# Kernel optimization log

Hardware: AMD Instinct MI355X
Metric: run time of the kernel (lower is better)

The kernel has to match this reference:

```python
import jax, jax.numpy as jnp
import numpy as np

B, S, D, H = 2, 2048, 1024, 16
DK = D // H  # 64

def setup_inputs() -> dict:
    key = jax.random.key(0)
    ks = jax.random.split(key, 8)
    xavier = np.sqrt(6.0 / (D + D))  # xavier_uniform bound for square Linear
    def lin_w(k):
        return jax.random.uniform(k, (D, D), jnp.float32, -xavier, xavier)
    return {
        'Q': jax.random.normal(ks[0], (B, S, D), jnp.float32),
        'length': jax.random.randint(ks[1], (B,), 1, S + 1, jnp.int32),
        'Wq': lin_w(ks[2]), 'bq': jnp.zeros((D,), jnp.float32),
        'Wk': lin_w(ks[3]), 'bk': jnp.zeros((D,), jnp.float32),
        'Wv': lin_w(ks[4]), 'bv': jnp.zeros((D,), jnp.float32),
    }

def reference(Q, length, Wq, bq, Wk, bk, Wv, bv):
    # project and split heads: [B,S,D] -> [B,H,S,DK]
    def heads(x, W, b):
        y = jnp.einsum('bsd,de->bse', x, W) + b
        return y.reshape(B, S, H, DK).transpose(0, 2, 1, 3)
    q = heads(Q, Wq, bq)
    k = heads(Q, Wk, bk)
    v = heads(Q, Wv, bv)
    scores = jnp.einsum('bhqd,bhkd->bhqk', q, k) / np.sqrt(DK)
    scores = jnp.exp(scores)  # NOTE: raw exp, no max-subtraction (faithful)
    # multiplicative key mask: mask[b,k] = k < length[b], broadcast over q,h
    mask = (jnp.arange(S)[None, :] < length[:, None]).astype(scores.dtype)
    scores = scores * mask[:, None, None, :]
    attn = scores / (jnp.sum(scores, axis=-1, keepdims=True) + 1e-8)
    ctx = jnp.einsum('bhqk,bhkd->bhqd', attn, v)
    return ctx.transpose(0, 2, 1, 3).reshape(B, S, D)
```

## Files before the change

### kernel.cpp

```cpp
#include <hip/hip_runtime.h>
#include <hip/hip_bf16.h>

#define B_  2
#define S_  2048
#define D_  1024
#define H_  16
#define DK_ 64
#define M_  (B_ * S_)

typedef short short8 __attribute__((ext_vector_type(8)));
typedef float float4v __attribute__((ext_vector_type(4)));

#define QSCALE 0.18033688011112042f

static __device__ __forceinline__ ushort f32_to_bf16bits(float f) {
    union { __hip_bfloat16 h; ushort u; } cv;
    cv.h = __float2bfloat16(f);
    return cv.u;
}

static __device__ __forceinline__ void glds16(const ushort* g, ushort* l) {
    __builtin_amdgcn_global_load_lds(
        (const __attribute__((address_space(1))) unsigned int*)g,
        (__attribute__((address_space(3))) unsigned int*)l, 16, 0, 0);
}

__global__ __launch_bounds__(256) void prep(
    const float* __restrict__ X, const float* __restrict__ W0,
    const float* __restrict__ W1, const float* __restrict__ W2,
    ushort* __restrict__ Xb, ushort* __restrict__ Wt)
{
    const int z = blockIdx.z;
    const int t = threadIdx.x;

    if (z >= 3) {
        const int blk = (z - 3) * 256 + blockIdx.y * 16 + blockIdx.x;
        const int i = blk * 2048 + t * 8;
        float4v a = *(const float4v*)(X + i);
        float4v b = *(const float4v*)(X + i + 4);
        short8 o;
        o[0] = (short)f32_to_bf16bits(a[0]); o[1] = (short)f32_to_bf16bits(a[1]);
        o[2] = (short)f32_to_bf16bits(a[2]); o[3] = (short)f32_to_bf16bits(a[3]);
        o[4] = (short)f32_to_bf16bits(b[0]); o[5] = (short)f32_to_bf16bits(b[1]);
        o[6] = (short)f32_to_bf16bits(b[2]); o[7] = (short)f32_to_bf16bits(b[3]);
        *(short8*)(Xb + i) = o;
        return;
    }

    const float* W = (z == 0) ? W0 : ((z == 1) ? W1 : W2);
    ushort* out = Wt + (size_t)z * D_ * D_;

    __shared__ ushort tile[64 * 72];
    int n0 = blockIdx.x * 64, k0 = blockIdx.y * 64;
    int r = t >> 3, g = t & 7;

    #pragma unroll
    for (int p = 0; p < 2; ++p) {
        int rr = r + p * 32;
        const float* src = W + (size_t)(k0 + rr) * D_ + n0 + g * 8;
        float4v a = *(const float4v*)src;
        float4v b = *(const float4v*)(src + 4);
        short8 o;
        o[0] = (short)f32_to_bf16bits(a[0]); o[1] = (short)f32_to_bf16bits(a[1]);
        o[2] = (short)f32_to_bf16bits(a[2]); o[3] = (short)f32_to_bf16bits(a[3]);
        o[4] = (short)f32_to_bf16bits(b[0]); o[5] = (short)f32_to_bf16bits(b[1]);
        o[6] = (short)f32_to_bf16bits(b[2]); o[7] = (short)f32_to_bf16bits(b[3]);
        *(short8*)&tile[rr * 72 + g * 8] = o;
    }
    __syncthreads();
    #pragma unroll
    for (int p = 0; p < 2; ++p) {
        int rr = r + p * 32;
        short8 v;
        #pragma unroll
        for (int i = 0; i < 8; ++i)
            v[i] = (short)tile[(g * 8 + i) * 72 + rr];
        *(short8*)(out + (size_t)(n0 + rr) * D_ + k0 + g * 8) = v;
    }
}

__global__ __launch_bounds__(256, 2) void proj_gemm(
    const ushort* __restrict__ X,
    const ushort* __restrict__ Wt,
    const float* __restrict__ b0, const float* __restrict__ b1,
    const float* __restrict__ b2,
    const int* __restrict__ length,
    ushort* __restrict__ qkv)
{
    const int m0 = blockIdx.x * 64, n0 = blockIdx.y * 128;
    const int bidx = m0 >> 11;
    const int s0 = m0 & (S_ - 1);
    const bool kv = (s0 < length[bidx]);

    __shared__ __align__(16) ushort As[64 * 64];
    __shared__ __align__(16) ushort Bs[3][128 * 64];

    const int t = threadIdx.x;
    const int lane = t & 63, wid = t >> 6;
    const int quad = lane >> 4, l16 = lane & 15;
    const int wr = wid >> 1, wc = wid & 1;

    float4v accq[2][4] = {}, acck[2][4] = {}, accv[2][4] = {};

    for (int kt = 0; kt < 16; ++kt) {
        const int k0 = kt * 64;
        __syncthreads();
        #pragma unroll
        for (int j = 0; j < 2; ++j) {
            const int cid = wid * 128 + j * 64 + lane;
            const int row = cid >> 3;
            const int cl  = (cid & 7) ^ (row & 7);
            glds16(X + (size_t)(m0 + row) * D_ + k0 + cl * 8, &As[cid * 8]);
        }
        #pragma unroll
        for (int j = 0; j < 4; ++j) {
            const int cid = wid * 256 + j * 64 + lane;
            const int row = cid >> 3;
            const int cl  = (cid & 7) ^ (row & 7);
            const size_t off = (size_t)(n0 + row) * D_ + k0 + cl * 8;
            glds16(Wt + off, &Bs[0][cid * 8]);
            if (kv) {
                glds16(Wt + (size_t)D_ * D_ + off,     &Bs[1][cid * 8]);
                glds16(Wt + (size_t)2 * D_ * D_ + off, &Bs[2][cid * 8]);
            }
        }
        __syncthreads();

        #pragma unroll
        for (int ks = 0; ks < 2; ++ks) {
            short8 a[2];
            #pragma unroll
            for (int i = 0; i < 2; ++i) {
                const int r = wr * 32 + i * 16 + l16;
                const int ph = (ks * 4 + quad) ^ (r & 7);
                a[i] = *(short8*)&As[r * 64 + ph * 8];
            }
            short8 bq[4];
            #pragma unroll
            for (int j = 0; j < 4; ++j) {
                const int r = wc * 64 + j * 16 + l16;
                const int ph = (ks * 4 + quad) ^ (r & 7);
                bq[j] = *(short8*)&Bs[0][r * 64 + ph * 8];
            }
            #pragma unroll
            for (int i = 0; i < 2; ++i)
                #pragma unroll
                for (int j = 0; j < 4; ++j)
                    accq[i][j] = __builtin_amdgcn_mfma_f32_16x16x32_bf16(
                        a[i], bq[j], accq[i][j], 0, 0, 0);
            if (kv) {
                short8 bk[4], bv[4];
                #pragma unroll
                for (int j = 0; j < 4; ++j) {
                    const int r = wc * 64 + j * 16 + l16;
                    const int ph = (ks * 4 + quad) ^ (r & 7);
                    bk[j] = *(short8*)&Bs[1][r * 64 + ph * 8];
                    bv[j] = *(short8*)&Bs[2][r * 64 + ph * 8];
                }
                #pragma unroll
                for (int i = 0; i < 2; ++i)
                    #pragma unroll
                    for (int j = 0; j < 4; ++j) {
                        acck[i][j] = __builtin_amdgcn_mfma_f32_16x16x32_bf16(
                            a[i], bk[j], acck[i][j], 0, 0, 0);
                        accv[i][j] = __builtin_amdgcn_mfma_f32_16x16x32_bf16(
                            a[i], bv[j], accv[i][j], 0, 0, 0);
                    }
            }
        }
    }

    #pragma unroll
    for (int j = 0; j < 4; ++j) {
        const int col = n0 + wc * 64 + j * 16 + l16;
        const int h = col >> 6, dk = col & (DK_ - 1);
        const float bvq = b0[col], bvk = b1[col], bvv = b2[col];
        #pragma unroll
        for (int i = 0; i < 2; ++i) {
            #pragma unroll
            for (int rr = 0; rr < 4; ++rr) {
                const int row = m0 + wr * 32 + i * 16 + quad * 4 + rr;
                const int s = row & (S_ - 1);
                const size_t hdr = ((size_t)(bidx * H_ + h) * S_ + s) * DK_ + dk;
                qkv[hdr] = f32_to_bf16bits((accq[i][j][rr] + bvq) * QSCALE);
                if (kv) {
                    qkv[(size_t)M_ * D_ + hdr] =
                        f32_to_bf16bits(acck[i][j][rr] + bvk);
                    qkv[(size_t)2 * M_ * D_ +
                        ((size_t)(bidx * H_ + h) * DK_ + dk) * S_ + s] =
                        f32_to_bf16bits(accv[i][j][rr] + bvv);
                }
            }
        }
    }
}

__global__ __launch_bounds__(256, 3) void attention(
    const ushort* __restrict__ qkv, const int* __restrict__ length,
    float* __restrict__ out)
{
    const int b = blockIdx.z, h = blockIdx.y, q0 = blockIdx.x * 64;
    int len = length[b];
    if (len > S_) len = S_;
    if (len < 1) len = 1;
    const int nkt = (len + 63) >> 6;

    const ushort* qb = qkv + ((size_t)(b * H_ + h) * S_ + q0) * DK_;
    const ushort* kb = qkv + (size_t)M_ * D_ + (size_t)(b * H_ + h) * S_ * DK_;
    const ushort* vb = qkv + (size_t)2 * M_ * D_ + (size_t)(b * H_ + h) * DK_ * S_;

    __shared__ __align__(16) ushort Qs[64 * 64];
    __shared__ __align__(16) ushort Ks[2][64 * 64];
    __shared__ __align__(16) ushort Vs[2][64 * 64];
    __shared__ __align__(16) ushort Ps[64 * 64];

    const int t = threadIdx.x, lane = t & 63, wid = t >> 6;
    const int quad = lane >> 4, l16 = lane & 15;
    const int qrow = wid * 16 + l16;
    const int e8 = (l16 & 7) << 1;

    #pragma unroll
    for (int j = 0; j < 2; ++j) {
        const int cid = wid * 128 + j * 64 + lane;
        const int row = cid >> 3;
        const int cl  = (cid & 7) ^ (row & 7);
        glds16(qb + (size_t)row * DK_ + cl * 8, &Qs[cid * 8]);
        glds16(kb + (size_t)row * DK_ + cl * 8, &Ks[0][cid * 8]);
        glds16(vb + (size_t)row * S_ + cl * 8,  &Vs[0][cid * 8]);
    }
    __syncthreads();

    short8 qfrag[2];
    #pragma unroll
    for (int ks = 0; ks < 2; ++ks) {
        const int phb = (ks * 4 + quad) ^ (l16 & 7);
        qfrag[ks] = *(short8*)&Qs[qrow * 64 + phb * 8];
    }

    short8 ones8;
    #pragma unroll
    for (int i = 0; i < 8; ++i) ones8[i] = (short)0x3F80;

    float4v cacc[4] = {};
    float4v racc = {};

    for (int kt = 0; kt < nkt; ++kt) {
        const int cur = kt & 1, nxt = cur ^ 1;
        if (kt + 1 < nkt) {
            #pragma unroll
            for (int j = 0; j < 2; ++j) {
                const int cid = wid * 128 + j * 64 + lane;
                const int row = cid >> 3;
                const int cl  = (cid & 7) ^ (row & 7);
                glds16(kb + (size_t)((kt + 1) * 64 + row) * DK_ + cl * 8,
                       &Ks[nxt][cid * 8]);
                glds16(vb + (size_t)row * S_ + (kt + 1) * 64 + cl * 8,
                       &Vs[nxt][cid * 8]);
            }
        }

        float4v sacc[4] = {};
        #pragma unroll
        for (int ks = 0; ks < 2; ++ks) {
            #pragma unroll
            for (int ct = 0; ct < 4; ++ct) {
                const int krow = ct * 16 + l16;
                const int pha = (ks * 4 + quad) ^ (krow & 7);
                short8 ak = *(short8*)&Ks[cur][krow * 64 + pha * 8];
                sacc[ct] = __builtin_amdgcn_mfma_f32_16x16x32_bf16(
                    ak, qfrag[ks], sacc[ct], 0, 0, 0);
            }
        }

        const bool full = ((kt + 1) * 64 <= len);
        #pragma unroll
        for (int ct = 0; ct < 4; ++ct) {
            float v0 = __builtin_amdgcn_exp2f(sacc[ct][0]);
            float v1 = __builtin_amdgcn_exp2f(sacc[ct][1]);
            float v2 = __builtin_amdgcn_exp2f(sacc[ct][2]);
            float v3 = __builtin_amdgcn_exp2f(sacc[ct][3]);
            if (!full) {
                const int kb0 = kt * 64 + ct * 16 + quad * 4;
                v0 = (kb0 + 0 < len) ? v0 : 0.f;
                v1 = (kb0 + 1 < len) ? v1 : 0.f;
                v2 = (kb0 + 2 < len) ? v2 : 0.f;
                v3 = (kb0 + 3 < len) ? v3 : 0.f;
            }
            uint2 w;
            w.x = (__float_as_uint(v0) >> 16) | (__float_as_uint(v1) & 0xFFFF0000u);
            w.y = (__float_as_uint(v2) >> 16) | (__float_as_uint(v3) & 0xFFFF0000u);
            const int c8 = (ct * 4 + quad) ^ e8;
            *(uint2*)&Ps[qrow * 64 + c8 * 4] = w;
        }

        #pragma unroll
        for (int ks = 0; ks < 2; ++ks) {
            const int pp = ((ks * 4 + quad) * 2) ^ e8;
            short8 ap = *(short8*)&Ps[qrow * 64 + pp * 4];
            #pragma unroll
            for (int ct = 0; ct < 4; ++ct) {
                const int vrow = ct * 16 + l16;
                const int phv = (ks * 4 + quad) ^ (vrow & 7);
                short8 vv = *(short8*)&Vs[cur][vrow * 64 + phv * 8];
                cacc[ct] = __builtin_amdgcn_mfma_f32_16x16x32_bf16(
                    ap, vv, cacc[ct], 0, 0, 0);
            }
            racc = __builtin_amdgcn_mfma_f32_16x16x32_bf16(
                ap, ones8, racc, 0, 0, 0);
        }
        __syncthreads();
    }

    #pragma unroll
    for (int rr = 0; rr < 4; ++rr) {
        const float inv = 1.0f / (racc[rr] + 1e-8f);
        const int q = q0 + wid * 16 + quad * 4 + rr;
        #pragma unroll
        for (int ct = 0; ct < 4; ++ct) {
            const int d = h * 64 + ct * 16 + l16;
            out[((size_t)b * S_ + q) * D_ + d] = cacc[ct][rr] * inv;
        }
    }
}

extern "C" void kernel_launch(void* const* d_in, const int* in_sizes, int n_in,
                              void* d_out, int out_size, void* d_ws, size_t ws_size,
                              hipStream_t stream)
{
    const float* Q   = (const float*)d_in[0];
    const int*   len = (const int*)d_in[1];
    const float* Wq  = (const float*)d_in[2];
    const float* bq  = (const float*)d_in[3];
    const float* Wk  = (const float*)d_in[4];
    const float* bk  = (const float*)d_in[5];
    const float* Wv  = (const float*)d_in[6];
    const float* bv  = (const float*)d_in[7];
    float* out = (float*)d_out;

    ushort* ws  = (ushort*)d_ws;
    ushort* Xb  = ws;
    ushort* Wt  = ws + (size_t)M_ * D_;
    ushort* qkv = Wt + (size_t)3 * D_ * D_;

    dim3 gPr(16, 16, 11);
    prep<<<gPr, 256, 0, stream>>>(Q, Wq, Wk, Wv, Xb, Wt);

    dim3 gP(M_ / 64, D_ / 128);
    proj_gemm<<<gP, 256, 0, stream>>>(Xb, Wt, bq, bk, bv, len, qkv);

    dim3 gA(S_ / 64, H_, B_);
    attention<<<gA, 256, 0, stream>>>(qkv, len, out);
}
```

Measured before the change: 156.2 us.

## Shrink projection tiles, alias Q/P shared memory, and interleave attention grid order

```diff
diff --git a/kernel.cpp b/kernel.cpp
--- a/kernel.cpp
+++ b/kernel.cpp
@@ -79,7 +79,7 @@
     }
 }
 
-__global__ __launch_bounds__(256, 2) void proj_gemm(
+__global__ __launch_bounds__(256, 4) void proj_gemm(
     const ushort* __restrict__ X,
     const ushort* __restrict__ Wt,
     const float* __restrict__ b0, const float* __restrict__ b1,
@@ -87,20 +87,22 @@
     const int* __restrict__ length,
     ushort* __restrict__ qkv)
 {
-    const int m0 = blockIdx.x * 64, n0 = blockIdx.y * 128;
+    const int bx = blockIdx.x;
+    const int m0 = (bx & 63) * 64;
+    const int n0 = (bx >> 6) * 64;
     const int bidx = m0 >> 11;
     const int s0 = m0 & (S_ - 1);
     const bool kv = (s0 < length[bidx]);
 
     __shared__ __align__(16) ushort As[64 * 64];
-    __shared__ __align__(16) ushort Bs[3][128 * 64];
+    __shared__ __align__(16) ushort Bs[3][64 * 64];
 
     const int t = threadIdx.x;
     const int lane = t & 63, wid = t >> 6;
     const int quad = lane >> 4, l16 = lane & 15;
     const int wr = wid >> 1, wc = wid & 1;
 
-    float4v accq[2][4] = {}, acck[2][4] = {}, accv[2][4] = {};
+    float4v accq[2][2] = {}, acck[2][2] = {}, accv[2][2] = {};
 
     for (int kt = 0; kt < 16; ++kt) {
         const int k0 = kt * 64;
@@ -111,12 +113,6 @@
             const int row = cid >> 3;
             const int cl  = (cid & 7) ^ (row & 7);
             glds16(X + (size_t)(m0 + row) * D_ + k0 + cl * 8, &As[cid * 8]);
-        }
-        #pragma unroll
-        for (int j = 0; j < 4; ++j) {
-            const int cid = wid * 256 + j * 64 + lane;
-            const int row = cid >> 3;
-            const int cl  = (cid & 7) ^ (row & 7);
             const size_t off = (size_t)(n0 + row) * D_ + k0 + cl * 8;
             glds16(Wt + off, &Bs[0][cid * 8]);
             if (kv) {
@@ -135,24 +131,24 @@
                 const int ph = (ks * 4 + quad) ^ (r & 7);
                 a[i] = *(short8*)&As[r * 64 + ph * 8];
             }
-            short8 bq[4];
-            #pragma unroll
-            for (int j = 0; j < 4; ++j) {
-                const int r = wc * 64 + j * 16 + l16;
+            short8 bq[2];
+            #pragma unroll
+            for (int j = 0; j < 2; ++j) {
+                const int r = wc * 32 + j * 16 + l16;
                 const int ph = (ks * 4 + quad) ^ (r & 7);
                 bq[j] = *(short8*)&Bs[0][r * 64 + ph * 8];
             }
             #pragma unroll
             for (int i = 0; i < 2; ++i)
                 #pragma unroll
-                for (int j = 0; j < 4; ++j)
+                for (int j = 0; j < 2; ++j)
                     accq[i][j] = __builtin_amdgcn_mfma_f32_16x16x32_bf16(
                         a[i], bq[j], accq[i][j], 0, 0, 0);
             if (kv) {
-                short8 bk[4], bv[4];
+                short8 bk[2], bv[2];
                 #pragma unroll
-                for (int j = 0; j < 4; ++j) {
-                    const int r = wc * 64 + j * 16 + l16;
+                for (int j = 0; j < 2; ++j) {
+                    const int r = wc * 32 + j * 16 + l16;
                     const int ph = (ks * 4 + quad) ^ (r & 7);
                     bk[j] = *(short8*)&Bs[1][r * 64 + ph * 8];
                     bv[j] = *(short8*)&Bs[2][r * 64 + ph * 8];
@@ -160,7 +156,7 @@
                 #pragma unroll
                 for (int i = 0; i < 2; ++i)
                     #pragma unroll
-                    for (int j = 0; j < 4; ++j) {
+                    for (int j = 0; j < 2; ++j) {
                         acck[i][j] = __builtin_amdgcn_mfma_f32_16x16x32_bf16(
                             a[i], bk[j], acck[i][j], 0, 0, 0);
                         accv[i][j] = __builtin_amdgcn_mfma_f32_16x16x32_bf16(
@@ -171,8 +167,8 @@
     }
 
     #pragma unroll
-    for (int j = 0; j < 4; ++j) {
-        const int col = n0 + wc * 64 + j * 16 + l16;
+    for (int j = 0; j < 2; ++j) {
+        const int col = n0 + wc * 32 + j * 16 + l16;
         const int h = col >> 6, dk = col & (DK_ - 1);
         const float bvq = b0[col], bvk = b1[col], bvv = b2[col];
         #pragma unroll
@@ -195,11 +191,12 @@
     }
 }
 
-__global__ __launch_bounds__(256, 3) void attention(
+__global__ __launch_bounds__(256, 4) void attention(
     const ushort* __restrict__ qkv, const int* __restrict__ length,
     float* __restrict__ out)
 {
-    const int b = blockIdx.z, h = blockIdx.y, q0 = blockIdx.x * 64;
+    const int bx = blockIdx.x;
+    const int b = bx & 1, h = (bx >> 1) & 15, q0 = (bx >> 5) * 64;
     int len = length[b];
     if (len > S_) len = S_;
     if (len < 1) len = 1;
@@ -209,10 +206,9 @@
     const ushort* kb = qkv + (size_t)M_ * D_ + (size_t)(b * H_ + h) * S_ * DK_;
     const ushort* vb = qkv + (size_t)2 * M_ * D_ + (size_t)(b * H_ + h) * DK_ * S_;
 
-    __shared__ __align__(16) ushort Qs[64 * 64];
+    __shared__ __align__(16) ushort QPs[64 * 64];
     __shared__ __align__(16) ushort Ks[2][64 * 64];
     __shared__ __align__(16) ushort Vs[2][64 * 64];
-    __shared__ __align__(16) ushort Ps[64 * 64];
 
     const int t = threadIdx.x, lane = t & 63, wid = t >> 6;
     const int quad = lane >> 4, l16 = lane & 15;
@@ -224,7 +220,7 @@
         const int cid = wid * 128 + j * 64 + lane;
         const int row = cid >> 3;
         const int cl  = (cid & 7) ^ (row & 7);
-        glds16(qb + (size_t)row * DK_ + cl * 8, &Qs[cid * 8]);
+        glds16(qb + (size_t)row * DK_ + cl * 8, &QPs[cid * 8]);
         glds16(kb + (size_t)row * DK_ + cl * 8, &Ks[0][cid * 8]);
         glds16(vb + (size_t)row * S_ + cl * 8,  &Vs[0][cid * 8]);
     }
@@ -234,7 +230,7 @@
     #pragma unroll
     for (int ks = 0; ks < 2; ++ks) {
         const int phb = (ks * 4 + quad) ^ (l16 & 7);
-        qfrag[ks] = *(short8*)&Qs[qrow * 64 + phb * 8];
+        qfrag[ks] = *(short8*)&QPs[qrow * 64 + phb * 8];
     }
 
     short8 ones8;
@@ -290,13 +286,13 @@
             w.x = (__float_as_uint(v0) >> 16) | (__float_as_uint(v1) & 0xFFFF0000u);
             w.y = (__float_as_uint(v2) >> 16) | (__float_as_uint(v3) & 0xFFFF0000u);
             const int c8 = (ct * 4 + quad) ^ e8;
-            *(uint2*)&Ps[qrow * 64 + c8 * 4] = w;
+            *(uint2*)&QPs[qrow * 64 + c8 * 4] = w;
         }
 
         #pragma unroll
         for (int ks = 0; ks < 2; ++ks) {
             const int pp = ((ks * 4 + quad) * 2) ^ e8;
-            short8 ap = *(short8*)&Ps[qrow * 64 + pp * 4];
+            short8 ap = *(short8*)&QPs[qrow * 64 + pp * 4];
             #pragma unroll
             for (int ct = 0; ct < 4; ++ct) {
                 const int vrow = ct * 16 + l16;
@@ -345,9 +341,7 @@
     dim3 gPr(16, 16, 11);
     prep<<<gPr, 256, 0, stream>>>(Q, Wq, Wk, Wv, Xb, Wt);
 
-    dim3 gP(M_ / 64, D_ / 128);
-    proj_gemm<<<gP, 256, 0, stream>>>(Xb, Wt, bq, bk, bv, len, qkv);
-
-    dim3 gA(S_ / 64, H_, B_);
-    attention<<<gA, 256, 0, stream>>>(qkv, len, out);
-}
+    proj_gemm<<<dim3(64 * 16), 256, 0, stream>>>(Xb, Wt, bq, bk, bv, len, qkv);
+
+    attention<<<dim3(2 * 16 * 32), 256, 0, stream>>>(qkv, len, out);
+}
```

New measurement: 166.2 us. 6.5% more time.

## Use 128-query tiles with 32x32x16 MFMA in attention kernel

Applied to the files above, without the earlier changes.

```diff
diff --git a/kernel.cpp b/kernel.cpp
--- a/kernel.cpp
+++ b/kernel.cpp
@@ -10,6 +10,7 @@
 
 typedef short short8 __attribute__((ext_vector_type(8)));
 typedef float float4v __attribute__((ext_vector_type(4)));
+typedef float float16v __attribute__((ext_vector_type(16)));
 
 #define QSCALE 0.18033688011112042f
 
@@ -195,11 +196,11 @@
     }
 }
 
-__global__ __launch_bounds__(256, 3) void attention(
+__global__ __launch_bounds__(256, 2) void attention(
     const ushort* __restrict__ qkv, const int* __restrict__ length,
     float* __restrict__ out)
 {
-    const int b = blockIdx.z, h = blockIdx.y, q0 = blockIdx.x * 64;
+    const int b = blockIdx.z, h = blockIdx.y, q0 = blockIdx.x * 128;
     int len = length[b];
     if (len > S_) len = S_;
     if (len < 1) len = 1;
@@ -209,40 +210,47 @@
     const ushort* kb = qkv + (size_t)M_ * D_ + (size_t)(b * H_ + h) * S_ * DK_;
     const ushort* vb = qkv + (size_t)2 * M_ * D_ + (size_t)(b * H_ + h) * DK_ * S_;
 
-    __shared__ __align__(16) ushort Qs[64 * 64];
+    __shared__ __align__(16) ushort Qs[128 * 64];
     __shared__ __align__(16) ushort Ks[2][64 * 64];
     __shared__ __align__(16) ushort Vs[2][64 * 64];
-    __shared__ __align__(16) ushort Ps[64 * 64];
+    __shared__ __align__(16) ushort Ps[128 * 64];
 
     const int t = threadIdx.x, lane = t & 63, wid = t >> 6;
-    const int quad = lane >> 4, l16 = lane & 15;
-    const int qrow = wid * 16 + l16;
-    const int e8 = (l16 & 7) << 1;
-
+    const int l32 = lane & 31, lhi = lane >> 5;
+    const int qbase = wid * 32;
+    const int prow = qbase + l32;
+    const int swz = (prow & 7) << 1;
+
+    #pragma unroll
+    for (int j = 0; j < 4; ++j) {
+        const int cid = wid * 256 + j * 64 + lane;
+        const int row = cid >> 3;
+        const int cl  = (cid & 7) ^ (row & 7);
+        glds16(qb + (size_t)row * DK_ + cl * 8, &Qs[cid * 8]);
+    }
     #pragma unroll
     for (int j = 0; j < 2; ++j) {
         const int cid = wid * 128 + j * 64 + lane;
         const int row = cid >> 3;
         const int cl  = (cid & 7) ^ (row & 7);
-        glds16(qb + (size_t)row * DK_ + cl * 8, &Qs[cid * 8]);
         glds16(kb + (size_t)row * DK_ + cl * 8, &Ks[0][cid * 8]);
         glds16(vb + (size_t)row * S_ + cl * 8,  &Vs[0][cid * 8]);
     }
     __syncthreads();
 
-    short8 qfrag[2];
-    #pragma unroll
-    for (int ks = 0; ks < 2; ++ks) {
-        const int phb = (ks * 4 + quad) ^ (l16 & 7);
-        qfrag[ks] = *(short8*)&Qs[qrow * 64 + phb * 8];
+    short8 qfrag[4];
+    #pragma unroll
+    for (int ks = 0; ks < 4; ++ks) {
+        const int ph = (ks * 2 + lhi) ^ (prow & 7);
+        qfrag[ks] = *(short8*)&Qs[prow * 64 + ph * 8];
     }
 
     short8 ones8;
     #pragma unroll
     for (int i = 0; i < 8; ++i) ones8[i] = (short)0x3F80;
 
-    float4v cacc[4] = {};
-    float4v racc = {};
+    float16v cacc[2] = {};
+    float16v racc = {};
 
     for (int kt = 0; kt < nkt; ++kt) {
         const int cur = kt & 1, nxt = cur ^ 1;
@@ -259,66 +267,76 @@
             }
         }
 
-        float4v sacc[4] = {};
-        #pragma unroll
-        for (int ks = 0; ks < 2; ++ks) {
-            #pragma unroll
-            for (int ct = 0; ct < 4; ++ct) {
-                const int krow = ct * 16 + l16;
-                const int pha = (ks * 4 + quad) ^ (krow & 7);
-                short8 ak = *(short8*)&Ks[cur][krow * 64 + pha * 8];
-                sacc[ct] = __builtin_amdgcn_mfma_f32_16x16x32_bf16(
-                    ak, qfrag[ks], sacc[ct], 0, 0, 0);
-            }
+        float16v sacc[2] = {};
+        #pragma unroll
+        for (int ks = 0; ks < 4; ++ks) {
+            const int ph = (ks * 2 + lhi) ^ (l32 & 7);
+            short8 ak0 = *(short8*)&Ks[cur][ l32       * 64 + ph * 8];
+            short8 ak1 = *(short8*)&Ks[cur][(l32 + 32) * 64 + ph * 8];
+            sacc[0] = __builtin_amdgcn_mfma_f32_32x32x16_bf16(
+                ak0, qfrag[ks], sacc[0], 0, 0, 0);
+            sacc[1] = __builtin_amdgcn_mfma_f32_32x32x16_bf16(
+                ak1, qfrag[ks], sacc[1], 0, 0, 0);
         }
 
         const bool full = ((kt + 1) * 64 <= len);
         #pragma unroll
-        for (int ct = 0; ct < 4; ++ct) {
-            float v0 = __builtin_amdgcn_exp2f(sacc[ct][0]);
-            float v1 = __builtin_amdgcn_exp2f(sacc[ct][1]);
-            float v2 = __builtin_amdgcn_exp2f(sacc[ct][2]);
-            float v3 = __builtin_amdgcn_exp2f(sacc[ct][3]);
-            if (!full) {
-                const int kb0 = kt * 64 + ct * 16 + quad * 4;
-                v0 = (kb0 + 0 < len) ? v0 : 0.f;
-                v1 = (kb0 + 1 < len) ? v1 : 0.f;
-                v2 = (kb0 + 2 < len) ? v2 : 0.f;
-                v3 = (kb0 + 3 < len) ? v3 : 0.f;
-            }
-            uint2 w;
-            w.x = (__float_as_uint(v0) >> 16) | (__float_as_uint(v1) & 0xFFFF0000u);
-            w.y = (__float_as_uint(v2) >> 16) | (__float_as_uint(v3) & 0xFFFF0000u);
-            const int c8 = (ct * 4 + quad) ^ e8;
-            *(uint2*)&Ps[qrow * 64 + c8 * 4] = w;
-        }
-
-        #pragma unroll
-        for (int ks = 0; ks < 2; ++ks) {
-            const int pp = ((ks * 4 + quad) * 2) ^ e8;
-            short8 ap = *(short8*)&Ps[qrow * 64 + pp * 4];
-            #pragma unroll
-            for (int ct = 0; ct < 4; ++ct) {
-                const int vrow = ct * 16 + l16;
-                const int phv = (ks * 4 + quad) ^ (vrow & 7);
-                short8 vv = *(short8*)&Vs[cur][vrow * 64 + phv * 8];
-                cacc[ct] = __builtin_amdgcn_mfma_f32_16x16x32_bf16(
-                    ap, vv, cacc[ct], 0, 0, 0);
-            }
-            racc = __builtin_amdgcn_mfma_f32_16x16x32_bf16(
-                ap, ones8, racc, 0, 0, 0);
+        for (int ktile = 0; ktile < 2; ++ktile) {
+            #pragma unroll
+            for (int g = 0; g < 4; ++g) {
+                float v0 = __builtin_amdgcn_exp2f(sacc[ktile][4 * g + 0]);
+                float v1 = __builtin_amdgcn_exp2f(sacc[ktile][4 * g + 1]);
+                float v2 = __builtin_amdgcn_exp2f(sacc[ktile][4 * g + 2]);
+                float v3 = __builtin_amdgcn_exp2f(sacc[ktile][4 * g + 3]);
+                if (!full) {
+                    const int kb0 = kt * 64 + ktile * 32 + 4 * lhi + 8 * g;
+                    v0 = (kb0 + 0 < len) ? v0 : 0.f;
+                    v1 = (kb0 + 1 < len) ? v1 : 0.f;
+                    v2 = (kb0 + 2 < len) ? v2 : 0.f;
+                    v3 = (kb0 + 3 < len) ? v3 : 0.f;
+                }
+                uint2 w;
+                w.x = (__float_as_uint(v0) >> 16) | (__float_as_uint(v1) & 0xFFFF0000u);
+                w.y = (__float_as_uint(v2) >> 16) | (__float_as_uint(v3) & 0xFFFF0000u);
+                const int c8 = (ktile * 8 + 2 * g + lhi) ^ swz;
+                *(uint2*)&Ps[prow * 64 + c8 * 4] = w;
+            }
+        }
+
+        short8 ap[4];
+        #pragma unroll
+        for (int ks = 0; ks < 4; ++ks) {
+            const int p = ((ks * 2 + lhi) * 2) ^ swz;
+            ap[ks] = *(short8*)&Ps[prow * 64 + p * 4];
+        }
+        #pragma unroll
+        for (int ks = 0; ks < 4; ++ks) {
+            #pragma unroll
+            for (int nt = 0; nt < 2; ++nt) {
+                const int vrow = nt * 32 + l32;
+                const int ph = (ks * 2 + lhi) ^ (vrow & 7);
+                short8 vv = *(short8*)&Vs[cur][vrow * 64 + ph * 8];
+                cacc[nt] = __builtin_amdgcn_mfma_f32_32x32x16_bf16(
+                    ap[ks], vv, cacc[nt], 0, 0, 0);
+            }
+            racc = __builtin_amdgcn_mfma_f32_32x32x16_bf16(
+                ap[ks], ones8, racc, 0, 0, 0);
         }
         __syncthreads();
     }
 
     #pragma unroll
-    for (int rr = 0; rr < 4; ++rr) {
-        const float inv = 1.0f / (racc[rr] + 1e-8f);
-        const int q = q0 + wid * 16 + quad * 4 + rr;
-        #pragma unroll
-        for (int ct = 0; ct < 4; ++ct) {
-            const int d = h * 64 + ct * 16 + l16;
-            out[((size_t)b * S_ + q) * D_ + d] = cacc[ct][rr] * inv;
+    for (int g = 0; g < 4; ++g) {
+        #pragma unroll
+        for (int i = 0; i < 4; ++i) {
+            const int reg = 4 * g + i;
+            const float inv = 1.0f / (racc[reg] + 1e-8f);
+            const int q = q0 + qbase + 4 * lhi + 8 * g + i;
+            #pragma unroll
+            for (int nt = 0; nt < 2; ++nt) {
+                const int d = h * 64 + nt * 32 + l32;
+                out[((size_t)b * S_ + q) * D_ + d] = cacc[nt][reg] * inv;
+            }
         }
     }
 }
@@ -348,6 +366,6 @@
     dim3 gP(M_ / 64, D_ / 128);
     proj_gemm<<<gP, 256, 0, stream>>>(Xb, Wt, bq, bk, bv, len, qkv);
 
-    dim3 gA(S_ / 64, H_, B_);
+    dim3 gA(S_ / 128, H_, B_);
     attention<<<gA, 256, 0, stream>>>(qkv, len, out);
 }
```

Result: slower. 162.4 us (+4.0%).

## Process 128 query rows per attention block to reuse K/V tiles

Applied to the files above, without the earlier changes.

```diff
diff --git a/kernel.cpp b/kernel.cpp
--- a/kernel.cpp
+++ b/kernel.cpp
@@ -199,7 +199,7 @@
     const ushort* __restrict__ qkv, const int* __restrict__ length,
     float* __restrict__ out)
 {
-    const int b = blockIdx.z, h = blockIdx.y, q0 = blockIdx.x * 64;
+    const int b = blockIdx.z, h = blockIdx.y, q0 = blockIdx.x * 128;
     int len = length[b];
     if (len > S_) len = S_;
     if (len < 1) len = 1;
@@ -209,40 +209,47 @@
     const ushort* kb = qkv + (size_t)M_ * D_ + (size_t)(b * H_ + h) * S_ * DK_;
     const ushort* vb = qkv + (size_t)2 * M_ * D_ + (size_t)(b * H_ + h) * DK_ * S_;
 
-    __shared__ __align__(16) ushort Qs[64 * 64];
+    __shared__ __align__(16) ushort QPs[128 * 64];
     __shared__ __align__(16) ushort Ks[2][64 * 64];
     __shared__ __align__(16) ushort Vs[2][64 * 64];
-    __shared__ __align__(16) ushort Ps[64 * 64];
 
     const int t = threadIdx.x, lane = t & 63, wid = t >> 6;
     const int quad = lane >> 4, l16 = lane & 15;
-    const int qrow = wid * 16 + l16;
     const int e8 = (l16 & 7) << 1;
 
+    #pragma unroll
+    for (int j = 0; j < 4; ++j) {
+        const int cid = wid * 256 + j * 64 + lane;
+        const int row = cid >> 3;
+        const int cl  = (cid & 7) ^ (row & 7);
+        glds16(qb + (size_t)row * DK_ + cl * 8, &QPs[cid * 8]);
+    }
     #pragma unroll
     for (int j = 0; j < 2; ++j) {
         const int cid = wid * 128 + j * 64 + lane;
         const int row = cid >> 3;
         const int cl  = (cid & 7) ^ (row & 7);
-        glds16(qb + (size_t)row * DK_ + cl * 8, &Qs[cid * 8]);
         glds16(kb + (size_t)row * DK_ + cl * 8, &Ks[0][cid * 8]);
         glds16(vb + (size_t)row * S_ + cl * 8,  &Vs[0][cid * 8]);
     }
     __syncthreads();
 
-    short8 qfrag[2];
-    #pragma unroll
-    for (int ks = 0; ks < 2; ++ks) {
-        const int phb = (ks * 4 + quad) ^ (l16 & 7);
-        qfrag[ks] = *(short8*)&Qs[qrow * 64 + phb * 8];
-    }
+    short8 qfrag[2][2];
+    #pragma unroll
+    for (int st = 0; st < 2; ++st)
+        #pragma unroll
+        for (int ks = 0; ks < 2; ++ks) {
+            const int qrow = wid * 32 + st * 16 + l16;
+            const int ph = (ks * 4 + quad) ^ (qrow & 7);
+            qfrag[st][ks] = *(short8*)&QPs[qrow * 64 + ph * 8];
+        }
 
     short8 ones8;
     #pragma unroll
     for (int i = 0; i < 8; ++i) ones8[i] = (short)0x3F80;
 
-    float4v cacc[4] = {};
-    float4v racc = {};
+    float4v cacc[2][4] = {};
+    float4v racc[2] = {};
 
     for (int kt = 0; kt < nkt; ++kt) {
         const int cur = kt & 1, nxt = cur ^ 1;
@@ -259,68 +266,86 @@
             }
         }
 
-        float4v sacc[4] = {};
-        #pragma unroll
-        for (int ks = 0; ks < 2; ++ks) {
+        float4v sacc[2][4] = {};
+        #pragma unroll
+        for (int ks = 0; ks < 2; ++ks)
             #pragma unroll
             for (int ct = 0; ct < 4; ++ct) {
                 const int krow = ct * 16 + l16;
                 const int pha = (ks * 4 + quad) ^ (krow & 7);
                 short8 ak = *(short8*)&Ks[cur][krow * 64 + pha * 8];
-                sacc[ct] = __builtin_amdgcn_mfma_f32_16x16x32_bf16(
-                    ak, qfrag[ks], sacc[ct], 0, 0, 0);
-            }
-        }
+                #pragma unroll
+                for (int st = 0; st < 2; ++st)
+                    sacc[st][ct] = __builtin_amdgcn_mfma_f32_16x16x32_bf16(
+                        ak, qfrag[st][ks], sacc[st][ct], 0, 0, 0);
+            }
 
         const bool full = ((kt + 1) * 64 <= len);
         #pragma unroll
-        for (int ct = 0; ct < 4; ++ct) {
-            float v0 = __builtin_amdgcn_exp2f(sacc[ct][0]);
-            float v1 = __builtin_amdgcn_exp2f(sacc[ct][1]);
-            float v2 = __builtin_amdgcn_exp2f(sacc[ct][2]);
-            float v3 = __builtin_amdgcn_exp2f(sacc[ct][3]);
-            if (!full) {
-                const int kb0 = kt * 64 + ct * 16 + quad * 4;
-                v0 = (kb0 + 0 < len) ? v0 : 0.f;
-                v1 = (kb0 + 1 < len) ? v1 : 0.f;
-                v2 = (kb0 + 2 < len) ? v2 : 0.f;
-                v3 = (kb0 + 3 < len) ? v3 : 0.f;
-            }
-            uint2 w;
-            w.x = (__float_as_uint(v0) >> 16) | (__float_as_uint(v1) & 0xFFFF0000u);
-            w.y = (__float_as_uint(v2) >> 16) | (__float_as_uint(v3) & 0xFFFF0000u);
-            const int c8 = (ct * 4 + quad) ^ e8;
-            *(uint2*)&Ps[qrow * 64 + c8 * 4] = w;
-        }
-
+        for (int st = 0; st < 2; ++st) {
+            const int qrow = wid * 32 + st * 16 + l16;
+            #pragma unroll
+            for (int ct = 0; ct < 4; ++ct) {
+                float v0 = __builtin_amdgcn_exp2f(sacc[st][ct][0]);
+                float v1 = __builtin_amdgcn_exp2f(sacc[st][ct][1]);
+                float v2 = __builtin_amdgcn_exp2f(sacc[st][ct][2]);
+                float v3 = __builtin_amdgcn_exp2f(sacc[st][ct][3]);
+                if (!full) {
+                    const int kb0 = kt * 64 + ct * 16 + quad * 4;
+                    v0 = (kb0 + 0 < len) ? v0 : 0.f;
+                    v1 = (kb0 + 1 < len) ? v1 : 0.f;
+                    v2 = (kb0 + 2 < len) ? v2 : 0.f;
+                    v3 = (kb0 + 3 < len) ? v3 : 0.f;
+                }
+                uint2 w;
+                w.x = (__float_as_uint(v0) >> 16) | (__float_as_uint(v1) & 0xFFFF0000u);
+                w.y = (__float_as_uint(v2) >> 16) | (__float_as_uint(v3) & 0xFFFF0000u);
+                const int c8 = (ct * 4 + quad) ^ e8;
+                *(uint2*)&QPs[qrow * 64 + c8 * 4] = w;
+            }
+        }
+
+        short8 ap[2][2];
+        #pragma unroll
+        for (int st = 0; st < 2; ++st)
+            #pragma unroll
+            for (int ks = 0; ks < 2; ++ks) {
+                const int qrow = wid * 32 + st * 16 + l16;
+                const int pp = ((ks * 4 + quad) * 2) ^ e8;
+                ap[st][ks] = *(short8*)&QPs[qrow * 64 + pp * 4];
+            }
         #pragma unroll
         for (int ks = 0; ks < 2; ++ks) {
-            const int pp = ((ks * 4 + quad) * 2) ^ e8;
-            short8 ap = *(short8*)&Ps[qrow * 64 + pp * 4];
             #pragma unroll
             for (int ct = 0; ct < 4; ++ct) {
                 const int vrow = ct * 16 + l16;
                 const int phv = (ks * 4 + quad) ^ (vrow & 7);
                 short8 vv = *(short8*)&Vs[cur][vrow * 64 + phv * 8];
-                cacc[ct] = __builtin_amdgcn_mfma_f32_16x16x32_bf16(
-                    ap, vv, cacc[ct], 0, 0, 0);
-            }
-            racc = __builtin_amdgcn_mfma_f32_16x16x32_bf16(
-                ap, ones8, racc, 0, 0, 0);
+                #pragma unroll
+                for (int st = 0; st < 2; ++st)
+                    cacc[st][ct] = __builtin_amdgcn_mfma_f32_16x16x32_bf16(
+                        ap[st][ks], vv, cacc[st][ct], 0, 0, 0);
+            }
+            #pragma unroll
+            for (int st = 0; st < 2; ++st)
+                racc[st] = __builtin_amdgcn_mfma_f32_16x16x32_bf16(
+                    ap[st][ks], ones8, racc[st], 0, 0, 0);
         }
         __syncthreads();
     }
 
     #pragma unroll
-    for (int rr = 0; rr < 4; ++rr) {
-        const float inv = 1.0f / (racc[rr] + 1e-8f);
-        const int q = q0 + wid * 16 + quad * 4 + rr;
-        #pragma unroll
-        for (int ct = 0; ct < 4; ++ct) {
-            const int d = h * 64 + ct * 16 + l16;
-            out[((size_t)b * S_ + q) * D_ + d] = cacc[ct][rr] * inv;
-        }
-    }
+    for (int st = 0; st < 2; ++st)
+        #pragma unroll
+        for (int rr = 0; rr < 4; ++rr) {
+            const float inv = 1.0f / (racc[st][rr] + 1e-8f);
+            const int q = q0 + wid * 32 + st * 16 + quad * 4 + rr;
+            #pragma unroll
+            for (int ct = 0; ct < 4; ++ct) {
+                const int d = h * 64 + ct * 16 + l16;
+                out[((size_t)b * S_ + q) * D_ + d] = cacc[st][ct][rr] * inv;
+            }
+        }
 }
 
 extern "C" void kernel_launch(void* const* d_in, const int* in_sizes, int n_in,
@@ -348,6 +373,6 @@
     dim3 gP(M_ / 64, D_ / 128);
     proj_gemm<<<gP, 256, 0, stream>>>(Xb, Wt, bq, bk, bv, len, qkv);
 
-    dim3 gA(S_ / 64, H_, B_);
+    dim3 gA(S_ / 128, H_, B_);
     attention<<<gA, 256, 0, stream>>>(qkv, len, out);
 }
```

Result: slower. 162.0 us (+3.7%).
